# Optimization experiments

Hardware: AMD Instinct MI355X
Metric: run time of the kernel (lower is better)

The kernel has to match this reference:

```python
import jax, jax.numpy as jnp
import numpy as np

B, D, OUT = 256, 63, 128
DP = D + 1  # 64


def setup_inputs() -> dict:
    key = jax.random.key(0)
    k1, k2, k3, k4, k5 = jax.random.split(key, 5)
    return {
        "x": jax.random.normal(k1, (B, D), dtype=jnp.float32),
        "protein_output": jax.random.normal(k2, (B, D), dtype=jnp.float32),
        "dynamic_output": jax.random.normal(k3, (B, D), dtype=jnp.float32),
        "W": jax.random.normal(k4, (DP ** 3, OUT), dtype=jnp.float32) * 0.02,
        "b": jax.random.normal(k5, (OUT,), dtype=jnp.float32) * 0.02,
    }


def reference(x, protein_output, dynamic_output, W, b):
    bsz = x.shape[0]
    ones = jnp.ones((bsz, 1), dtype=x.dtype)
    a = jnp.concatenate([x, ones], axis=1)               # [B, D+1]
    p = jnp.concatenate([protein_output, ones], axis=1)   # [B, D+1]
    d = jnp.concatenate([dynamic_output, ones], axis=1)   # [B, D+1]
    # rank-1 trilinear outer product, flattened row-major: idx = (i*(D+1)+j)*(D+1)+k
    ab = jnp.einsum('bi,bj->bij', a, p)                   # [B, D+1, D+1]
    abc = jnp.einsum('bij,bk->bijk', ab, d)               # [B, D+1, D+1, D+1]
    feat = abc.reshape(bsz, -1)                           # [B, (D+1)^3]
    return feat @ W + b                                   # [B, OUT]
```

## Files before the change

### kernel.cpp

```cpp
#include <hip/hip_runtime.h>
#include <hip/hip_bf16.h>

typedef __attribute__((ext_vector_type(8))) short short8v;
typedef __attribute__((ext_vector_type(4))) float floatx4;

__device__ __forceinline__ unsigned int pkbf(float a, float b) {
  __hip_bfloat162 h = __float22bfloat162_rn(make_float2(a, b));
  union { __hip_bfloat162 h; unsigned int u; } c; c.h = h;
  return c.u;
}

__global__ void bias_init(const float* __restrict__ bias, float* __restrict__ out) {
  int idx = blockIdx.x * 256 + threadIdx.x;
  out[idx] = bias[idx & 127];
}

__global__ __launch_bounds__(512, 2)
void tfn_gemm(const float* __restrict__ X, const float* __restrict__ P,
              const float* __restrict__ Dyn, const float* __restrict__ W,
              float* __restrict__ out) {
  __shared__ float p_lds[16][256];

  const int tid = threadIdx.x;
  const int wv = tid >> 6, lane = tid & 63;
  const int q = lane >> 4, l16 = lane & 15;
  const int r = wv & 3;
  const int cg = wv >> 2;

  const int c = blockIdx.x;
  const int i = c >> 2;
  const int j0 = (c & 3) << 4;
  const long gk0 = (long)c << 10;

  for (int idx = tid; idx < 256 * 16; idx += 512) {
    int bb = idx >> 4, jj = idx & 15;
    int j = j0 + jj;
    p_lds[jj][bb] = (j < 63) ? P[bb * 63 + j] : 1.0f;
  }

  float e[4][2][8];
  #pragma unroll
  for (int rt = 0; rt < 4; ++rt) {
    int brow = (r << 6) + (rt << 4) + l16;
    float av = (i < 63) ? X[brow * 63 + i] : 1.0f;
    #pragma unroll
    for (int h = 0; h < 2; ++h) {
      int kb = (h << 5) + (q << 3);
      #pragma unroll
      for (int t = 0; t < 8; ++t) {
        int k = kb + t;
        float dv = (k < 63) ? Dyn[brow * 63 + k] : 1.0f;
        e[rt][h][t] = av * dv;
      }
    }
  }

  floatx4 acc[4][4];
  #pragma unroll
  for (int a = 0; a < 4; ++a)
    #pragma unroll
    for (int b = 0; b < 4; ++b) acc[a][b] = (floatx4)0.0f;

  __syncthreads();

  const float* wstep = W + (gk0 + (q << 3)) * 128 + (cg << 6) + l16;
  const float* wp0 = wstep;
  const float* wp1 = wstep + 4096;

  float wf0[4][8], wf1[4][8];

  #pragma unroll
  for (int nt = 0; nt < 4; ++nt)
    #pragma unroll
    for (int t = 0; t < 8; ++t) {
      wf0[nt][t] = wp0[t * 128 + nt * 16];
      wf1[nt][t] = wp1[t * 128 + nt * 16];
    }

#define FA_MFMA(h, fbv)                                                         \
  {                                                                             \
    union { short8v v; unsigned int u[4]; } fa[4];                              \
    _Pragma("unroll") for (int rt = 0; rt < 4; ++rt)                            \
        _Pragma("unroll") for (int v2 = 0; v2 < 4; ++v2)                        \
            fa[rt].u[v2] = pkbf(pb[rt] * e[rt][h][2 * v2],                      \
                                pb[rt] * e[rt][h][2 * v2 + 1]);                 \
    _Pragma("unroll") for (int rt = 0; rt < 4; ++rt)                            \
        _Pragma("unroll") for (int nt = 0; nt < 4; ++nt)                        \
            acc[rt][nt] = __builtin_amdgcn_mfma_f32_16x16x32_bf16(              \
                fa[rt].v, (fbv)[nt].v, acc[rt][nt], 0, 0, 0);                   \
  }

  for (int jj = 0; jj < 16; ++jj) {
    float pb[4];
    #pragma unroll
    for (int rt = 0; rt < 4; ++rt)
      pb[rt] = p_lds[jj][(r << 6) + (rt << 4) + l16];

    union { short8v v; unsigned int u[4]; } fb0[4];
    #pragma unroll
    for (int nt = 0; nt < 4; ++nt)
      #pragma unroll
      for (int v2 = 0; v2 < 4; ++v2)
        fb0[nt].u[v2] = pkbf(wf0[nt][2 * v2], wf0[nt][2 * v2 + 1]);
    if (jj < 15) {
      const float* np = wp0 + 8192;
      #pragma unroll
      for (int nt = 0; nt < 4; ++nt)
        #pragma unroll
        for (int t = 0; t < 8; ++t)
          wf0[nt][t] = np[t * 128 + nt * 16];
    }
    FA_MFMA(0, fb0)

    union { short8v v; unsigned int u[4]; } fb1[4];
    #pragma unroll
    for (int nt = 0; nt < 4; ++nt)
      #pragma unroll
      for (int v2 = 0; v2 < 4; ++v2)
        fb1[nt].u[v2] = pkbf(wf1[nt][2 * v2], wf1[nt][2 * v2 + 1]);
    if (jj < 15) {
      const float* np = wp1 + 8192;
      #pragma unroll
      for (int nt = 0; nt < 4; ++nt)
        #pragma unroll
        for (int t = 0; t < 8; ++t)
          wf1[nt][t] = np[t * 128 + nt * 16];
    }
    FA_MFMA(1, fb1)

    wp0 += 8192;
    wp1 += 8192;
  }
#undef FA_MFMA

  #pragma unroll
  for (int rt0 = 0; rt0 < 4; ++rt0) {
    #pragma unroll
    for (int nt0 = 0; nt0 < 4; ++nt0) {
      const int rt = (rt0 + (c >> 2)) & 3;
      const int nt = (nt0 + c) & 3;
      int col = (cg << 6) + (nt << 4) + l16;
      #pragma unroll
      for (int g = 0; g < 4; ++g) {
        int brow = (r << 6) + (rt << 4) + (q << 2) + g;
        atomicAdd(&out[brow * 128 + col], acc[rt][nt][g]);
      }
    }
  }
}

extern "C" void kernel_launch(void* const* d_in, const int* in_sizes, int n_in,
                              void* d_out, int out_size, void* d_ws, size_t ws_size,
                              hipStream_t stream) {
  const float* x   = (const float*)d_in[0];
  const float* p   = (const float*)d_in[1];
  const float* dyn = (const float*)d_in[2];
  const float* W   = (const float*)d_in[3];
  const float* b   = (const float*)d_in[4];
  float* out = (float*)d_out;

  bias_init<<<128, 256, 0, stream>>>(b, out);
  tfn_gemm<<<256, 512, 0, stream>>>(x, p, dyn, W, out);
}
```

Before: 251.9 us.

## Stage W tiles through double-buffered LDS with global_load_lds

Loads of W now go directly from global memory into LDS through global_load_lds, into two padded buffers that are double-buffered. Each half-step prefetches the next 32-row tile while fragments are read from LDS, where before each lane issued strided global loads into registers. The aim is to cut register pressure and give coalesced row loads. In exchange it adds a __syncthreads per half-step and extra LDS traffic. Synchronisation of the async LDS writes relies only on the barrier, with no explicit vmcnt wait, which could be fragile.

```diff
diff --git a/kernel.cpp b/kernel.cpp
--- a/kernel.cpp
+++ b/kernel.cpp
@@ -4,10 +4,18 @@
 typedef __attribute__((ext_vector_type(8))) short short8v;
 typedef __attribute__((ext_vector_type(4))) float floatx4;
 
+#define LROW 130
+
 __device__ __forceinline__ unsigned int pkbf(float a, float b) {
   __hip_bfloat162 h = __float22bfloat162_rn(make_float2(a, b));
   union { __hip_bfloat162 h; unsigned int u; } c; c.h = h;
   return c.u;
+}
+
+__device__ __forceinline__ void glds4(const float* g, float* l) {
+  __builtin_amdgcn_global_load_lds(
+      (const __attribute__((address_space(1))) void*)g,
+      (__attribute__((address_space(3))) void*)l, 4, 0, 0);
 }
 
 __global__ void bias_init(const float* __restrict__ bias, float* __restrict__ out) {
@@ -19,6 +27,7 @@
 void tfn_gemm(const float* __restrict__ X, const float* __restrict__ P,
               const float* __restrict__ Dyn, const float* __restrict__ W,
               float* __restrict__ out) {
+  __shared__ float Wl[2][32 * LROW];
   __shared__ float p_lds[16][256];
 
   const int tid = threadIdx.x;
@@ -61,25 +70,33 @@
     #pragma unroll
     for (int b = 0; b < 4; ++b) acc[a][b] = (floatx4)0.0f;
 
+#define STAGE(sN, buf)                                                          \
+  {                                                                             \
+    const long krow = gk0 + ((long)(sN) << 5) + (wv << 2);                      \
+    _Pragma("unroll") for (int rr = 0; rr < 4; ++rr)                            \
+        _Pragma("unroll") for (int h2 = 0; h2 < 2; ++h2)                        \
+            glds4(W + (krow + rr) * 128 + (h2 << 6) + lane,                     \
+                  &Wl[buf][((wv << 2) + rr) * LROW + (h2 << 6)]);               \
+  }
+
+  STAGE(0, 0)
   __syncthreads();
 
-  const float* wstep = W + (gk0 + (q << 3)) * 128 + (cg << 6) + l16;
-  const float* wp0 = wstep;
-  const float* wp1 = wstep + 4096;
+  const int foff = ((q << 3) * LROW) + (cg << 6) + l16;
 
-  float wf0[4][8], wf1[4][8];
-
-  #pragma unroll
-  for (int nt = 0; nt < 4; ++nt)
-    #pragma unroll
-    for (int t = 0; t < 8; ++t) {
-      wf0[nt][t] = wp0[t * 128 + nt * 16];
-      wf1[nt][t] = wp1[t * 128 + nt * 16];
-    }
-
-#define FA_MFMA(h, fbv)                                                         \
+#define HALFSTEP(jj, h)                                                         \
   {                                                                             \
-    union { short8v v; unsigned int u[4]; } fa[4];                              \
+    const int s = ((jj) << 1) | (h);                                            \
+    if (s < 31) STAGE(s + 1, 1 - (h))                                           \
+    float wf[4][8];                                                             \
+    const float* fr = &Wl[h][foff];                                             \
+    _Pragma("unroll") for (int nt = 0; nt < 4; ++nt)                            \
+        _Pragma("unroll") for (int t = 0; t < 8; ++t)                           \
+            wf[nt][t] = fr[t * LROW + nt * 16];                                 \
+    union { short8v v; unsigned int u[4]; } fb[4], fa[4];                       \
+    _Pragma("unroll") for (int nt = 0; nt < 4; ++nt)                            \
+        _Pragma("unroll") for (int v2 = 0; v2 < 4; ++v2)                        \
+            fb[nt].u[v2] = pkbf(wf[nt][2 * v2], wf[nt][2 * v2 + 1]);            \
     _Pragma("unroll") for (int rt = 0; rt < 4; ++rt)                            \
         _Pragma("unroll") for (int v2 = 0; v2 < 4; ++v2)                        \
             fa[rt].u[v2] = pkbf(pb[rt] * e[rt][h][2 * v2],                      \
@@ -87,7 +104,8 @@
     _Pragma("unroll") for (int rt = 0; rt < 4; ++rt)                            \
         _Pragma("unroll") for (int nt = 0; nt < 4; ++nt)                        \
             acc[rt][nt] = __builtin_amdgcn_mfma_f32_16x16x32_bf16(              \
-                fa[rt].v, (fbv)[nt].v, acc[rt][nt], 0, 0, 0);                   \
+                fa[rt].v, fb[nt].v, acc[rt][nt], 0, 0, 0);                      \
+    __syncthreads();                                                            \
   }
 
   for (int jj = 0; jj < 16; ++jj) {
@@ -95,43 +113,11 @@
     #pragma unroll
     for (int rt = 0; rt < 4; ++rt)
       pb[rt] = p_lds[jj][(r << 6) + (rt << 4) + l16];
-
-    union { short8v v; unsigned int u[4]; } fb0[4];
-    #pragma unroll
-    for (int nt = 0; nt < 4; ++nt)
-      #pragma unroll
-      for (int v2 = 0; v2 < 4; ++v2)
-        fb0[nt].u[v2] = pkbf(wf0[nt][2 * v2], wf0[nt][2 * v2 + 1]);
-    if (jj < 15) {
-      const float* np = wp0 + 8192;
-      #pragma unroll
-      for (int nt = 0; nt < 4; ++nt)
-        #pragma unroll
-        for (int t = 0; t < 8; ++t)
-          wf0[nt][t] = np[t * 128 + nt * 16];
-    }
-    FA_MFMA(0, fb0)
-
-    union { short8v v; unsigned int u[4]; } fb1[4];
-    #pragma unroll
-    for (int nt = 0; nt < 4; ++nt)
-      #pragma unroll
-      for (int v2 = 0; v2 < 4; ++v2)
-        fb1[nt].u[v2] = pkbf(wf1[nt][2 * v2], wf1[nt][2 * v2 + 1]);
-    if (jj < 15) {
-      const float* np = wp1 + 8192;
-      #pragma unroll
-      for (int nt = 0; nt < 4; ++nt)
-        #pragma unroll
-        for (int t = 0; t < 8; ++t)
-          wf1[nt][t] = np[t * 128 + nt * 16];
-    }
-    FA_MFMA(1, fb1)
-
-    wp0 += 8192;
-    wp1 += 8192;
+    HALFSTEP(jj, 0)
+    HALFSTEP(jj, 1)
   }
-#undef FA_MFMA
+#undef HALFSTEP
+#undef STAGE
 
   #pragma unroll
   for (int rt0 = 0; rt0 < 4; ++rt0) {
```

Measured after the change: 368.0 us. 46.1% more time.
